# Performance work log

Hardware: AMD Instinct MI355X
Metric: run time of the kernel (lower is better)

The kernel has to match this reference:

```python
import jax, jax.numpy as jnp
import numpy as np

DIM = 1280
NUM_HEADS = 16
HEAD_DIM = DIM // NUM_HEADS  # 80
HIDDEN = DIM * 4             # 5120
SEQ = 4096
EPS = 1e-6


def _layernorm(x, scale, bias):
    mu = jnp.mean(x, axis=-1, keepdims=True)
    var = jnp.mean((x - mu) ** 2, axis=-1, keepdims=True)
    return (x - mu) * jax.lax.rsqrt(var + EPS) * scale + bias


def _rotate_half(x):
    x1, x2 = jnp.split(x, 2, axis=-1)
    return jnp.concatenate([-x2, x1], axis=-1)


def _apply_rope(x, freqs):
    # x: [N, H, D], freqs: [N, D//2]
    orig = x.dtype
    x = x.astype(jnp.float32)
    cos = jnp.repeat(jnp.cos(freqs), 2, axis=-1)[:, None, :].astype(jnp.float32)  # [N,1,D]
    sin = jnp.repeat(jnp.sin(freqs), 2, axis=-1)[:, None, :].astype(jnp.float32)
    return (x * cos + _rotate_half(x) * sin).astype(orig)


def _quick_gelu(x):
    return x * jax.nn.sigmoid(1.702 * x)


def setup_inputs() -> dict:
    key = jax.random.key(0)
    ks = jax.random.split(key, 12)
    s = 0.02
    inp = {
        "hidden_states": jax.random.normal(ks[0], (SEQ, DIM), dtype=jnp.float32),
        "rotary_pos_emb": jax.random.normal(ks[1], (SEQ, HEAD_DIM // 2), dtype=jnp.float32),
        "cu_seqlens": jnp.array([0, 1024, 2048, 3072, 4096], dtype=jnp.int32),
        "w_qkv": jax.random.normal(ks[2], (DIM, 3 * DIM), dtype=jnp.float32) * s,
        "b_qkv": jnp.zeros((3 * DIM,), dtype=jnp.float32),
        "w_proj": jax.random.normal(ks[3], (DIM, DIM), dtype=jnp.float32) * s,
        "b_proj": jnp.zeros((DIM,), dtype=jnp.float32),
        "w_fc1": jax.random.normal(ks[4], (DIM, HIDDEN), dtype=jnp.float32) * s,
        "b_fc1": jnp.zeros((HIDDEN,), dtype=jnp.float32),
        "w_fc2": jax.random.normal(ks[5], (HIDDEN, DIM), dtype=jnp.float32) * s,
        "b_fc2": jnp.zeros((DIM,), dtype=jnp.float32),
        "ln1_scale": jnp.ones((DIM,), dtype=jnp.float32),
        "ln1_bias": jnp.zeros((DIM,), dtype=jnp.float32),
        "ln2_scale": jnp.ones((DIM,), dtype=jnp.float32),
        "ln2_bias": jnp.zeros((DIM,), dtype=jnp.float32),
    }
    return inp


def _attention(x, cu_seqlens, rotary_pos_emb, w_qkv, b_qkv, w_proj, b_proj):
    N = x.shape[0]
    qkv = (x @ w_qkv + b_qkv).reshape(N, 3, NUM_HEADS, HEAD_DIM)
    q, k, v = qkv[:, 0], qkv[:, 1], qkv[:, 2]  # each [N, H, D]
    q = _apply_rope(q, rotary_pos_emb)
    k = _apply_rope(k, rotary_pos_emb)
    # block-diagonal mask from cu_seqlens (faithful to original construction)
    row_ids = jnp.arange(N)[None, None, :]
    col_ids = jnp.arange(N)[None, :, None]
    starts = cu_seqlens[:-1][:, None, None]
    ends = cu_seqlens[1:][:, None, None]
    is_valid = (row_ids >= starts) & (row_ids < ends) & (col_ids >= starts) & (col_ids < ends)
    combined = jnp.any(is_valid, axis=0)  # [N, N]
    bias = jnp.where(combined, 0.0, jnp.finfo(q.dtype).min)
    scores = jnp.einsum("shd,thd->hst", q, k) / np.sqrt(HEAD_DIM).astype(np.float32)
    scores = scores + bias[None, :, :]
    probs = jax.nn.softmax(scores.astype(jnp.float32), axis=-1).astype(q.dtype)
    out = jnp.einsum("hst,thd->shd", probs, v).reshape(N, DIM)
    return out @ w_proj + b_proj


def reference(hidden_states, rotary_pos_emb, cu_seqlens, w_qkv, b_qkv, w_proj, b_proj,
              w_fc1, b_fc1, w_fc2, b_fc2, ln1_scale, ln1_bias, ln2_scale, ln2_bias):
    h = hidden_states
    h = h + _attention(_layernorm(h, ln1_scale, ln1_bias), cu_seqlens, rotary_pos_emb,
                       w_qkv, b_qkv, w_proj, b_proj)
    m = _layernorm(h, ln2_scale, ln2_bias)
    h = h + (_quick_gelu(m @ w_fc1 + b_fc1) @ w_fc2 + b_fc2)
    return h
```

## Files before the change

kernel.cpp:

```cpp
#include <hip/hip_runtime.h>
#include <hip/hip_bf16.h>
#include <math.h>

typedef __bf16 bf16;
typedef __bf16 bf16x8 __attribute__((ext_vector_type(8)));
typedef float f32x4 __attribute__((ext_vector_type(4)));

#define DIM 1280
#define SEQ 4096
#define NH 16
#define HD 80
#define HIDDEN 5120
#define FLAG_THRESH 4096

#define S_VMCNT(n) asm volatile("s_waitcnt vmcnt(" #n ")" ::: "memory")
#define S_LGKM0() asm volatile("s_waitcnt lgkmcnt(0)" ::: "memory")
#define S_BAR() __builtin_amdgcn_s_barrier()
#define SCHED0() __builtin_amdgcn_sched_barrier(0)

__device__ __forceinline__ void gl_lds16(const bf16* g, bf16* l) {
  __builtin_amdgcn_global_load_lds((const __attribute__((address_space(1))) void*)g,
                                   (__attribute__((address_space(3))) void*)l, 16, 0, 0);
}

__device__ __forceinline__ f32x4 fz4() { f32x4 v; v.x = 0.f; v.y = 0.f; v.z = 0.f; v.w = 0.f; return v; }

__device__ __forceinline__ float ldx(const void* p, size_t i, bool f32) {
  if (f32) return ((const float*)p)[i];
  return (float)((const bf16*)p)[i];
}

__global__ void zero_flag_k(int* flag) { *flag = 0; }

__global__ __launch_bounds__(256) void sniff_k(const unsigned short* h, int n, int* flag) {
  int i = blockIdx.x * 256 + threadIdx.x;
  int c = 0;
  for (int idx = i; idx < n; idx += 256 * gridDim.x) {
    int e = (h[idx] >> 7) & 0xFF;
    c += (e >= 0xC8) ? 1 : 0;
  }
  #pragma unroll
  for (int o = 32; o; o >>= 1) c += __shfl_down(c, o);
  if ((threadIdx.x & 63) == 0 && c) atomicAdd(flag, c);
}

__global__ __launch_bounds__(256) void transpose_k(const void* __restrict__ in, bf16* __restrict__ out,
                                                   int R, int C, const int* __restrict__ flag) {
  bool f32 = *flag > FLAG_THRESH;
  __shared__ bf16 tile[32][33];
  int c0 = blockIdx.x * 32, r0 = blockIdx.y * 32;
  int tx = threadIdx.x, ty = threadIdx.y;
  #pragma unroll
  for (int i = 0; i < 4; i++)
    tile[ty + 8 * i][tx] = (bf16)ldx(in, (size_t)(r0 + ty + 8 * i) * C + c0 + tx, f32);
  __syncthreads();
  #pragma unroll
  for (int i = 0; i < 4; i++)
    out[(size_t)(c0 + ty + 8 * i) * R + r0 + tx] = tile[tx][ty + 8 * i];
}

__global__ __launch_bounds__(256) void ln_k(const void* __restrict__ x, const void* __restrict__ sc,
                                            const void* __restrict__ bi, bf16* __restrict__ out,
                                            const int* __restrict__ flag, int force_f32) {
  bool pf32 = *flag > FLAG_THRESH;
  bool xf32 = force_f32 || pf32;
  int row = blockIdx.x, t = threadIdx.x;
  float v[5];
  float s = 0.f, sq = 0.f;
  #pragma unroll
  for (int i = 0; i < 5; i++) {
    v[i] = ldx(x, (size_t)row * DIM + i * 256 + t, xf32);
    s += v[i]; sq += v[i] * v[i];
  }
  #pragma unroll
  for (int o = 32; o; o >>= 1) { s += __shfl_down(s, o); sq += __shfl_down(sq, o); }
  __shared__ float rs[4], rq[4];
  if ((t & 63) == 0) { rs[t >> 6] = s; rq[t >> 6] = sq; }
  __syncthreads();
  s = rs[0] + rs[1] + rs[2] + rs[3];
  sq = rq[0] + rq[1] + rq[2] + rq[3];
  float mean = s * (1.f / DIM);
  float var = sq * (1.f / DIM) - mean * mean;
  float rstd = rsqrtf(fmaxf(var, 0.f) + 1e-6f);
  #pragma unroll
  for (int i = 0; i < 5; i++) {
    int c = i * 256 + t;
    out[(size_t)row * DIM + c] = (bf16)((v[i] - mean) * rstd * ldx(sc, c, pf32) + ldx(bi, c, pf32));
  }
}

template <int TN>
__device__ __forceinline__ void gemm_step64(const bf16* As, const bf16* Bs, f32x4 (&acc)[4][TN],
                                            int wm, int wn, int quad, int l15) {
  int rsw = l15 & 7;
  #pragma unroll
  for (int ks = 0; ks < 2; ks++) {
    int csw = ((ks * 4 + quad) ^ rsw) * 8;
    bf16x8 af[4], bfr[TN];
    #pragma unroll
    for (int tm = 0; tm < 4; tm++) af[tm] = *(const bf16x8*)&As[(wm + tm * 16 + l15) * 64 + csw];
    #pragma unroll
    for (int tn = 0; tn < TN; tn++) bfr[tn] = *(const bf16x8*)&Bs[(wn + tn * 16 + l15) * 64 + csw];
    #pragma unroll
    for (int tm = 0; tm < 4; tm++)
      #pragma unroll
      for (int tn = 0; tn < TN; tn++)
        acc[tm][tn] = __builtin_amdgcn_mfma_f32_16x16x32_bf16(af[tm], bfr[tn], acc[tm][tn], 0, 0, 0);
  }
}

template <int MODE, int NT>
__global__ __launch_bounds__(256) void gemm_bt(const bf16* __restrict__ A, const bf16* __restrict__ Bt,
                                               const void* __restrict__ bias, const void* __restrict__ res,
                                               void* __restrict__ out, int M, int N, int K,
                                               const int* __restrict__ flag) {
  bool pf32 = *flag > FLAG_THRESH;
  constexpr int TN = NT / 32;
  constexpr int NB = NT / 32;
  __shared__ bf16 As0[128 * 64];
  __shared__ bf16 As1[128 * 64];
  __shared__ bf16 Bs0[NT * 64];
  __shared__ bf16 Bs1[NT * 64];
  int tid = threadIdx.x;
  int lane = tid & 63, wv = tid >> 6;
  int quad = lane >> 4, l15 = lane & 15;
  int m0 = blockIdx.y * 128, n0 = blockIdx.x * NT;
  int wm = (wv & 1) * 64, wn = (wv >> 1) * (NT / 2);
  const bf16* Ag = A + (size_t)m0 * K;
  const bf16* Bg = Bt + (size_t)n0 * K;
  int r0 = tid >> 3;
  int c0s = ((tid & 7) ^ ((tid >> 3) & 7)) * 8;
  f32x4 acc[4][TN];
  #pragma unroll
  for (int i = 0; i < 4; i++)
    #pragma unroll
    for (int j = 0; j < TN; j++) acc[i][j] = fz4();

#define STAGE_BT(as, bs, kk) do {                                                          \
    _Pragma("unroll")                                                                      \
    for (int j = 0; j < 4; j++)                                                            \
      gl_lds16(Ag + (size_t)(r0 + j * 32) * K + (kk) + c0s, &(as)[(tid + j * 256) * 8]);   \
    _Pragma("unroll")                                                                      \
    for (int j = 0; j < NB; j++)                                                           \
      gl_lds16(Bg + (size_t)(r0 + j * 32) * K + (kk) + c0s, &(bs)[(tid + j * 256) * 8]);   \
  } while (0)

  STAGE_BT(As0, Bs0, 0);
  for (int k0 = 0; k0 < K; k0 += 128) {
    STAGE_BT(As1, Bs1, k0 + 64);
    if constexpr (NT == 128) { S_VMCNT(8); } else { S_VMCNT(6); }
    S_BAR();
    gemm_step64<TN>(As0, Bs0, acc, wm, wn, quad, l15);
    S_BAR();
    if (k0 + 128 < K) {
      STAGE_BT(As0, Bs0, k0 + 128);
      if constexpr (NT == 128) { S_VMCNT(8); } else { S_VMCNT(6); }
    } else {
      S_VMCNT(0);
    }
    S_BAR();
    gemm_step64<TN>(As1, Bs1, acc, wm, wn, quad, l15);
    S_BAR();
  }
#undef STAGE_BT

  #pragma unroll
  for (int tm = 0; tm < 4; tm++) {
    #pragma unroll
    for (int tn = 0; tn < TN; tn++) {
      #pragma unroll
      for (int r = 0; r < 4; r++) {
        int row = m0 + wm + tm * 16 + quad * 4 + r;
        int col = n0 + wn + tn * 16 + l15;
        size_t idx = (size_t)row * N + col;
        float vv = acc[tm][tn][r] + ldx(bias, col, pf32);
        if constexpr (MODE == 0) ((bf16*)out)[idx] = (bf16)vv;
        if constexpr (MODE == 1) ((float*)out)[idx] = vv + ldx(res, idx, pf32);
        if constexpr (MODE == 2) ((bf16*)out)[idx] = (bf16)(vv / (1.f + __expf(-1.702f * vv)));
      }
    }
  }
}

__global__ __launch_bounds__(256) void gemm_sk(const bf16* __restrict__ A, const bf16* __restrict__ Bt,
                                               float* __restrict__ part, int M, int N, int K, int chunk) {
  __shared__ bf16 As0[128 * 64];
  __shared__ bf16 As1[128 * 64];
  __shared__ bf16 Bs0[64 * 64];
  __shared__ bf16 Bs1[64 * 64];
  int tid = threadIdx.x;
  int lane = tid & 63, wv = tid >> 6;
  int quad = lane >> 4, l15 = lane & 15;
  int m0 = blockIdx.y * 128, n0 = blockIdx.x * 64;
  int wm = (wv & 1) * 64, wn = (wv >> 1) * 32;
  int kb = blockIdx.z * chunk;
  const bf16* Ag = A + (size_t)m0 * K;
  const bf16* Bg = Bt + (size_t)n0 * K;
  int r0 = tid >> 3;
  int c0s = ((tid & 7) ^ ((tid >> 3) & 7)) * 8;
  f32x4 acc[4][2];
  #pragma unroll
  for (int i = 0; i < 4; i++)
    #pragma unroll
    for (int j = 0; j < 2; j++) acc[i][j] = fz4();

#define STAGE_SK(as, bs, kk) do {                                                          \
    _Pragma("unroll")                                                                      \
    for (int j = 0; j < 4; j++)                                                            \
      gl_lds16(Ag + (size_t)(r0 + j * 32) * K + (kk) + c0s, &(as)[(tid + j * 256) * 8]);   \
    _Pragma("unroll")                                                                      \
    for (int j = 0; j < 2; j++)                                                            \
      gl_lds16(Bg + (size_t)(r0 + j * 32) * K + (kk) + c0s, &(bs)[(tid + j * 256) * 8]);   \
  } while (0)

  STAGE_SK(As0, Bs0, kb);
  for (int k0 = kb; k0 < kb + chunk; k0 += 128) {
    STAGE_SK(As1, Bs1, k0 + 64);
    S_VMCNT(6);
    S_BAR();
    gemm_step64<2>(As0, Bs0, acc, wm, wn, quad, l15);
    S_BAR();
    if (k0 + 128 < kb + chunk) {
      STAGE_SK(As0, Bs0, k0 + 128);
      S_VMCNT(6);
    } else {
      S_VMCNT(0);
    }
    S_BAR();
    gemm_step64<2>(As1, Bs1, acc, wm, wn, quad, l15);
    S_BAR();
  }
#undef STAGE_SK

  float* po = part + (size_t)blockIdx.z * M * N;
  #pragma unroll
  for (int tm = 0; tm < 4; tm++) {
    #pragma unroll
    for (int tn = 0; tn < 2; tn++) {
      #pragma unroll
      for (int r = 0; r < 4; r++) {
        int row = m0 + wm + tm * 16 + quad * 4 + r;
        int col = n0 + wn + tn * 16 + l15;
        po[(size_t)row * N + col] = acc[tm][tn][r];
      }
    }
  }
}

__global__ __launch_bounds__(256) void reduce2_k(const float* __restrict__ p0, const float* __restrict__ p1,
                                                 const void* __restrict__ bias, const float* __restrict__ res,
                                                 float* __restrict__ out, int NCOL,
                                                 const int* __restrict__ flag) {
  bool pf32 = *flag > FLAG_THRESH;
  size_t i = ((size_t)blockIdx.x * 256 + threadIdx.x) * 4;
  int col = (int)(i % NCOL);
  float4 a = *(const float4*)&p0[i];
  float4 b = *(const float4*)&p1[i];
  float4 r = *(const float4*)&res[i];
  float4 o;
  o.x = a.x + b.x + r.x + ldx(bias, col + 0, pf32);
  o.y = a.y + b.y + r.y + ldx(bias, col + 1, pf32);
  o.z = a.z + b.z + r.z + ldx(bias, col + 2, pf32);
  o.w = a.w + b.w + r.w + ldx(bias, col + 3, pf32);
  *(float4*)&out[i] = o;
}

__global__ __launch_bounds__(256) void rope_k(bf16* __restrict__ qkv, const void* __restrict__ rot,
                                              const int* __restrict__ flag) {
  bool pf32 = *flag > FLAG_THRESH;
  int idx = blockIdx.x * 256 + threadIdx.x;
  int d = idx % 40;
  int t = idx / 40;
  int head = t & 15;
  int seq = t >> 4;
  float f1 = ldx(rot, (size_t)seq * 40 + (d >> 1), pf32);
  float f2 = ldx(rot, (size_t)seq * 40 + (d >> 1) + 20, pf32);
  float c1 = cosf(f1), s1 = sinf(f1), c2 = cosf(f2), s2 = sinf(f2);
  const float scq = 0.11180339887498949f;
  size_t base = (size_t)seq * (3 * DIM) + head * HD + d;
  float x1 = (float)qkv[base], x2 = (float)qkv[base + 40];
  qkv[base] = (bf16)((x1 * c1 - x2 * s1) * scq);
  qkv[base + 40] = (bf16)((x2 * c2 + x1 * s2) * scq);
  x1 = (float)qkv[base + DIM]; x2 = (float)qkv[base + DIM + 40];
  qkv[base + DIM] = (bf16)(x1 * c1 - x2 * s1);
  qkv[base + DIM + 40] = (bf16)(x2 * c2 + x1 * s2);
}

__global__ __launch_bounds__(256, 4) void attn_k(const bf16* __restrict__ qkv, const int* __restrict__ cu,
                                                 bf16* __restrict__ out) {
  __shared__ __align__(16) char smem[38144];
  bf16* Qs = (bf16*)smem;
  bf16* Ks = (bf16*)(smem + 13312);
  bf16* Vt = (bf16*)(smem + 26624);
  bf16* Ps = (bf16*)smem;
  int tid = threadIdx.x, lane = tid & 63, wv = tid >> 6;
  int quad = lane >> 4, l15 = lane & 15;
  int qt = blockIdx.x, head = blockIdx.y, seg = blockIdx.z;
  int s0 = cu[seg], s1 = cu[seg + 1];
  int q0 = s0 + qt * 64;
  if (q0 >= s1) return;
  const bf16* qh = qkv + head * HD;
  const bf16* kh = qkv + DIM + head * HD;
  const bf16* vh = qkv + 2 * DIM + head * HD;
  const int RS = 3 * DIM;
  uint4 z4; z4.x = 0; z4.y = 0; z4.z = 0; z4.w = 0;
  for (int i = tid; i < 128; i += 256) {
    int r = i >> 1, c = i & 1;
    *(uint4*)&Qs[r * 104 + 80 + c * 8] = z4;
    *(uint4*)&Ks[r * 104 + 80 + c * 8] = z4;
  }
  for (int i = tid; i < 640; i += 256) {
    int r = i / 10, c = i % 10;
    *(bf16x8*)&Qs[r * 104 + c * 8] = *(const bf16x8*)&qh[(size_t)(q0 + r) * RS + c * 8];
  }
  __syncthreads();
  bf16x8 aq[3];
  #pragma unroll
  for (int ks = 0; ks < 3; ks++)
    aq[ks] = *(const bf16x8*)&Qs[(wv * 16 + l15) * 104 + ks * 32 + quad * 8];

  int ir[3], ic8[3], vr[3], vc8[3];
  #pragma unroll
  for (int u = 0; u < 3; u++) {
    int i = tid + u * 256;
    ir[u] = i / 10; ic8[u] = (i % 10) * 8;
    vr[u] = i & 63; vc8[u] = (i >> 6) * 8;
  }
  bool act2 = tid < 128;

  bf16x8 kreg[3], vreg[3];
  #pragma unroll
  for (int u = 0; u < 3; u++)
    if (u < 2 || act2) {
      kreg[u] = *(const bf16x8*)&kh[(size_t)(s0 + ir[u]) * RS + ic8[u]];
      vreg[u] = *(const bf16x8*)&vh[(size_t)(s0 + vr[u]) * RS + vc8[u]];
    }

  float m_r[4], l_r[4];
  f32x4 oacc[5];
  #pragma unroll
  for (int r = 0; r < 4; r++) { m_r[r] = -1e30f; l_r[r] = 0.f; }
  #pragma unroll
  for (int nt = 0; nt < 5; nt++) oacc[nt] = fz4();

  for (int kt = s0; kt < s1; kt += 64) {
    S_BAR();
    SCHED0();
    #pragma unroll
    for (int u = 0; u < 3; u++)
      if (u < 2 || act2) {
        *(bf16x8*)&Ks[ir[u] * 104 + ic8[u]] = kreg[u];
        #pragma unroll
        for (int j = 0; j < 8; j++) Vt[(vc8[u] + j) * 72 + vr[u]] = vreg[u][j];
      }
    if (kt + 64 < s1) {
      #pragma unroll
      for (int u = 0; u < 3; u++)
        if (u < 2 || act2) {
          kreg[u] = *(const bf16x8*)&kh[(size_t)(kt + 64 + ir[u]) * RS + ic8[u]];
          vreg[u] = *(const bf16x8*)&vh[(size_t)(kt + 64 + vr[u]) * RS + vc8[u]];
        }
    }
    S_LGKM0();
    S_BAR();
    SCHED0();
    f32x4 sacc[4];
    #pragma unroll
    for (int j = 0; j < 4; j++) sacc[j] = fz4();
    __builtin_amdgcn_s_setprio(1);
    #pragma unroll
    for (int ks = 0; ks < 3; ks++) {
      #pragma unroll
      for (int j = 0; j < 4; j++) {
        bf16x8 bk = *(const bf16x8*)&Ks[(j * 16 + l15) * 104 + ks * 32 + quad * 8];
        sacc[j] = __builtin_amdgcn_mfma_f32_16x16x32_bf16(aq[ks], bk, sacc[j], 0, 0, 0);
      }
    }
    __builtin_amdgcn_s_setprio(0);
    #pragma unroll
    for (int r = 0; r < 4; r++) {
      float mx = fmaxf(fmaxf(sacc[0][r], sacc[1][r]), fmaxf(sacc[2][r], sacc[3][r]));
      #pragma unroll
      for (int o = 8; o; o >>= 1) mx = fmaxf(mx, __shfl_xor(mx, o));
      float mnew = fmaxf(m_r[r], mx);
      float alpha = __expf(m_r[r] - mnew);
      float psum = 0.f;
      #pragma unroll
      for (int j = 0; j < 4; j++) {
        float p = __expf(sacc[j][r] - mnew);
        psum += p;
        Ps[wv * 1152 + (quad * 4 + r) * 72 + j * 16 + l15] = (bf16)p;
      }
      #pragma unroll
      for (int o = 8; o; o >>= 1) psum += __shfl_xor(psum, o);
      l_r[r] = l_r[r] * alpha + psum;
      m_r[r] = mnew;
      #pragma unroll
      for (int nt = 0; nt < 5; nt++) oacc[nt][r] *= alpha;
    }
    __builtin_amdgcn_s_setprio(1);
    #pragma unroll
    for (int ks = 0; ks < 2; ks++) {
      bf16x8 ap = *(const bf16x8*)&Ps[wv * 1152 + l15 * 72 + ks * 32 + quad * 8];
      #pragma unroll
      for (int nt = 0; nt < 5; nt++) {
        bf16x8 bv = *(const bf16x8*)&Vt[(nt * 16 + l15) * 72 + ks * 32 + quad * 8];
        oacc[nt] = __builtin_amdgcn_mfma_f32_16x16x32_bf16(ap, bv, oacc[nt], 0, 0, 0);
      }
    }
    __builtin_amdgcn_s_setprio(0);
  }
  #pragma unroll
  for (int nt = 0; nt < 5; nt++) {
    #pragma unroll
    for (int r = 0; r < 4; r++) {
      int row = q0 + wv * 16 + quad * 4 + r;
      int d = nt * 16 + l15;
      out[(size_t)row * DIM + head * HD + d] = (bf16)(oacc[nt][r] / l_r[r]);
    }
  }
}

#define FLAG_OFF 0UL
#define QKVT_OFF 256UL
#define PROJT_OFF 9830656UL
#define FC1T_OFF 13107456UL
#define FC2T_OFF 26214656UL
#define LN_OFF 39321856UL
#define QKV_OFF 49807616UL
#define PART_OFF 49807616UL
#define AO_OFF 81264896UL
#define H1_OFF 91750656UL
#define FC1O_OFF 112722176UL

extern "C" void kernel_launch(void* const* d_in, const int* in_sizes, int n_in,
                              void* d_out, int out_size, void* d_ws, size_t ws_size,
                              hipStream_t stream) {
  const void* hidden = d_in[0];
  const void* rot    = d_in[1];
  const int*  cu     = (const int*)d_in[2];
  const void* w_qkv  = d_in[3];
  const void* b_qkv  = d_in[4];
  const void* w_proj = d_in[5];
  const void* b_proj = d_in[6];
  const void* w_fc1  = d_in[7];
  const void* b_fc1  = d_in[8];
  const void* w_fc2  = d_in[9];
  const void* b_fc2  = d_in[10];
  const void* ln1s   = d_in[11];
  const void* ln1b   = d_in[12];
  const void* ln2s   = d_in[13];
  const void* ln2b   = d_in[14];

  char* ws = (char*)d_ws;
  int* flag   = (int*)(ws + FLAG_OFF);
  bf16* qkvT  = (bf16*)(ws + QKVT_OFF);
  bf16* projT = (bf16*)(ws + PROJT_OFF);
  bf16* fc1T  = (bf16*)(ws + FC1T_OFF);
  bf16* fc2T  = (bf16*)(ws + FC2T_OFF);
  bf16* ln_bf = (bf16*)(ws + LN_OFF);
  bf16* qkv   = (bf16*)(ws + QKV_OFF);
  float* part = (float*)(ws + PART_OFF);
  bf16* ao    = (bf16*)(ws + AO_OFF);
  float* h1   = (float*)(ws + H1_OFF);
  bf16* fc1o  = (bf16*)(ws + FC1O_OFF);

  zero_flag_k<<<1, 1, 0, stream>>>(flag);
  sniff_k<<<256, 256, 0, stream>>>((const unsigned short*)hidden, SEQ * DIM, flag);

  dim3 tb(32, 8);
  transpose_k<<<dim3(120, 40), tb, 0, stream>>>(w_qkv, qkvT, 1280, 3840, flag);
  transpose_k<<<dim3(40, 40), tb, 0, stream>>>(w_proj, projT, 1280, 1280, flag);
  transpose_k<<<dim3(160, 40), tb, 0, stream>>>(w_fc1, fc1T, 1280, 5120, flag);
  transpose_k<<<dim3(40, 160), tb, 0, stream>>>(w_fc2, fc2T, 5120, 1280, flag);

  ln_k<<<SEQ, 256, 0, stream>>>(hidden, ln1s, ln1b, ln_bf, flag, 0);
  gemm_bt<0, 128><<<dim3(30, 32), 256, 0, stream>>>(ln_bf, qkvT, b_qkv, nullptr, qkv, SEQ, 3 * DIM, DIM, flag);
  rope_k<<<10240, 256, 0, stream>>>(qkv, rot, flag);
  attn_k<<<dim3(16, NH, 4), 256, 0, stream>>>(qkv, cu, ao);
  gemm_bt<1, 64><<<dim3(20, 32), 256, 0, stream>>>(ao, projT, b_proj, hidden, h1, SEQ, DIM, DIM, flag);
  ln_k<<<SEQ, 256, 0, stream>>>(h1, ln2s, ln2b, ln_bf, flag, 1);
  gemm_bt<2, 128><<<dim3(40, 32), 256, 0, stream>>>(ln_bf, fc1T, b_fc1, nullptr, fc1o, SEQ, HIDDEN, DIM, flag);
  gemm_sk<<<dim3(20, 32, 2), 256, 0, stream>>>(fc1o, fc2T, part, SEQ, DIM, HIDDEN, HIDDEN / 2);
  reduce2_k<<<SEQ * DIM / 1024, 256, 0, stream>>>(part, part + (size_t)SEQ * DIM, b_fc2, h1,
                                                  (float*)d_out, DIM, flag);
}
```

Before: 604.8 us.

## Add 256x256 eight-wave GEMM with multi-stage LDS pipeline for QKV and FC1

Introduces a new GEMM kernel using 256x256 output tiles with 512 threads (8 waves), a 16-slot LDS ring buffer fed by direct global-to-LDS loads, split half-tile compute phases interleaved with prefetches, and MFMA priority raising. It replaces the 128-wide gemm_bt for the QKV and FC1 projections to raise per-block data reuse and hide global load latency. Grids shrink to 240 and 320 blocks, which on a 256-CU device may leave poor wave-quantization balance; the large LDS footprint limits occupancy.

Result: no change. 594.6 us (-1.7%).

```diff
diff --git a/kernel.cpp b/kernel.cpp
--- a/kernel.cpp
+++ b/kernel.cpp
@@ -86,6 +86,99 @@
   for (int i = 0; i < 5; i++) {
     int c = i * 256 + t;
     out[(size_t)row * DIM + c] = (bf16)((v[i] - mean) * rstd * ldx(sc, c, pf32) + ldx(bi, c, pf32));
+  }
+}
+
+template <int MODE>
+__global__ __launch_bounds__(512, 2) void gemm256p8(const bf16* __restrict__ A, const bf16* __restrict__ Bt,
+                                                    const void* __restrict__ bias, void* __restrict__ out,
+                                                    int M, int N, int K, const int* __restrict__ flag) {
+  bool pf32 = *flag > FLAG_THRESH;
+  __shared__ bf16 lds[16][128 * 32];
+  int tid = threadIdx.x;
+  int lane = tid & 63, wv = tid >> 6;
+  int quad = lane >> 4, l15 = lane & 15;
+  int wm = wv >> 2, wn = wv & 3;
+  int m0 = blockIdx.y * 256, n0 = blockIdx.x * 256;
+  const bf16* Ag = A + (size_t)m0 * K;
+  const bf16* Bg = Bt + (size_t)n0 * K;
+  int r0 = tid >> 2;
+  int c0s = ((tid & 3) ^ ((tid >> 3) & 3)) * 8;
+  int csw = (quad ^ ((l15 >> 1) & 3)) * 8;
+  int bloc = (wn & 1) * 64;
+
+  f32x4 acc[8][4];
+  #pragma unroll
+  for (int i = 0; i < 8; i++)
+    #pragma unroll
+    for (int j = 0; j < 4; j++) acc[i][j] = fz4();
+
+#define STG(h) do { int _t = (h) >> 2, _p = (h) & 3;                                     \
+    const bf16* _g = ((_p) < 2 ? Ag : Bg) + (size_t)(((_p) & 1) * 128 + r0) * K + _t * 32 + c0s; \
+    gl_lds16(_g, &lds[(h) & 15][tid * 8]); } while (0)
+
+  int TK = K >> 5;
+  int HMAX = TK << 2;
+  #pragma unroll
+  for (int h = 0; h < 8; ++h) STG(h);
+  S_VMCNT(4);
+  SCHED0(); S_BAR(); SCHED0();
+
+  for (int T = 0; T < TK; ++T) {
+    const bf16* sA = lds[(4 * T + wm) & 15];
+    const bf16* sB = lds[(4 * T + 2 + (wn >> 1)) & 15];
+    int h0 = 4 * T + 8;
+    bf16x8 a[4], b[4];
+    #pragma unroll
+    for (int m = 0; m < 4; m++)
+      a[m] = *(const bf16x8*)&sA[(m * 16 + l15) * 32 + csw];
+    #pragma unroll
+    for (int n = 0; n < 4; n++)
+      b[n] = *(const bf16x8*)&sB[(bloc + n * 16 + l15) * 32 + csw];
+    if (h0 < HMAX) STG(h0);
+    if (h0 + 1 < HMAX) STG(h0 + 1);
+    SCHED0(); S_BAR(); SCHED0();
+    __builtin_amdgcn_s_setprio(1);
+    #pragma unroll
+    for (int m = 0; m < 4; m++)
+      #pragma unroll
+      for (int n = 0; n < 4; n++)
+        acc[m][n] = __builtin_amdgcn_mfma_f32_16x16x32_bf16(a[m], b[n], acc[m][n], 0, 0, 0);
+    __builtin_amdgcn_s_setprio(0);
+    SCHED0(); S_BAR();
+    #pragma unroll
+    for (int m = 0; m < 4; m++)
+      a[m] = *(const bf16x8*)&sA[((64 + m * 16 + l15)) * 32 + csw];
+    if (h0 + 2 < HMAX) STG(h0 + 2);
+    if (h0 + 3 < HMAX) STG(h0 + 3);
+    if (h0 + 3 < HMAX) { S_VMCNT(4); } else { S_VMCNT(0); }
+    SCHED0(); S_BAR(); SCHED0();
+    __builtin_amdgcn_s_setprio(1);
+    #pragma unroll
+    for (int m = 0; m < 4; m++)
+      #pragma unroll
+      for (int n = 0; n < 4; n++)
+        acc[4 + m][n] = __builtin_amdgcn_mfma_f32_16x16x32_bf16(a[m], b[n], acc[4 + m][n], 0, 0, 0);
+    __builtin_amdgcn_s_setprio(0);
+    SCHED0(); S_BAR();
+  }
+#undef STG
+
+  #pragma unroll
+  for (int n = 0; n < 4; n++) {
+    int col = n0 + wn * 64 + n * 16 + l15;
+    float bv = ldx(bias, col, pf32);
+    #pragma unroll
+    for (int m = 0; m < 8; m++) {
+      #pragma unroll
+      for (int r = 0; r < 4; r++) {
+        int row = m0 + wm * 128 + m * 16 + quad * 4 + r;
+        size_t idx = (size_t)row * N + col;
+        float vv = acc[m][n][r] + bv;
+        if constexpr (MODE == 0) ((bf16*)out)[idx] = (bf16)vv;
+        if constexpr (MODE == 2) ((bf16*)out)[idx] = (bf16)(vv / (1.f + __expf(-1.702f * vv)));
+      }
+    }
   }
 }
 
@@ -475,12 +568,12 @@
   transpose_k<<<dim3(40, 160), tb, 0, stream>>>(w_fc2, fc2T, 5120, 1280, flag);
 
   ln_k<<<SEQ, 256, 0, stream>>>(hidden, ln1s, ln1b, ln_bf, flag, 0);
-  gemm_bt<0, 128><<<dim3(30, 32), 256, 0, stream>>>(ln_bf, qkvT, b_qkv, nullptr, qkv, SEQ, 3 * DIM, DIM, flag);
+  gemm256p8<0><<<dim3(15, 16), 512, 0, stream>>>(ln_bf, qkvT, b_qkv, qkv, SEQ, 3 * DIM, DIM, flag);
   rope_k<<<10240, 256, 0, stream>>>(qkv, rot, flag);
   attn_k<<<dim3(16, NH, 4), 256, 0, stream>>>(qkv, cu, ao);
   gemm_bt<1, 64><<<dim3(20, 32), 256, 0, stream>>>(ao, projT, b_proj, hidden, h1, SEQ, DIM, DIM, flag);
   ln_k<<<SEQ, 256, 0, stream>>>(h1, ln2s, ln2b, ln_bf, flag, 1);
-  gemm_bt<2, 128><<<dim3(40, 32), 256, 0, stream>>>(ln_bf, fc1T, b_fc1, nullptr, fc1o, SEQ, HIDDEN, DIM, flag);
+  gemm256p8<2><<<dim3(20, 16), 512, 0, stream>>>(ln_bf, fc1T, b_fc1, fc1o, SEQ, HIDDEN, DIM, flag);
   gemm_sk<<<dim3(20, 32, 2), 256, 0, stream>>>(fc1o, fc2T, part, SEQ, DIM, HIDDEN, HIDDEN / 2);
   reduce2_k<<<SEQ * DIM / 1024, 256, 0, stream>>>(part, part + (size_t)SEQ * DIM, b_fc2, h1,
                                                   (float*)d_out, DIM, flag);
```
